# Kernel optimization log

Measured on AMD Instinct MI355X. Metric: run time of the kernel, lower is better.

## Reference

```python
import jax, jax.numpy as jnp
import numpy as np

T, B, U = 256, 4, 64
E_ENC, E_DEC, J, V = 1024, 640, 640, 4096
LN_EPS = 1e-5


def layer_norm(x, gamma, beta):
    mu = jnp.mean(x, axis=-1, keepdims=True)
    var = jnp.mean(jnp.square(x - mu), axis=-1, keepdims=True)
    return (x - mu) * jax.lax.rsqrt(var + LN_EPS) * gamma + beta


def setup_inputs() -> dict:
    key = jax.random.key(0)
    ks = jax.random.split(key, 8)
    inp = {
        "encoder_out": jax.random.normal(ks[0], (T, B, E_ENC), dtype=jnp.float32),
        "decoder_out": jax.random.normal(ks[1], (U, B, E_DEC), dtype=jnp.float32),
        # proj_encoder
        "W_enc": jax.random.normal(ks[2], (J, E_ENC), dtype=jnp.float32) * (E_ENC ** -0.5),
        "b_enc": jnp.zeros((J,), dtype=jnp.float32),
        "g_enc": jnp.ones((J,), dtype=jnp.float32),
        "be_enc": jnp.zeros((J,), dtype=jnp.float32),
        # proj_decoder
        "W_dec": jax.random.normal(ks[3], (J, E_DEC), dtype=jnp.float32) * (E_DEC ** -0.5),
        "b_dec": jnp.zeros((J,), dtype=jnp.float32),
        "g_dec": jnp.ones((J,), dtype=jnp.float32),
        "be_dec": jnp.zeros((J,), dtype=jnp.float32),
        # fc_out (init.normal_ with std = joint_dim**-0.5)
        "W_out": jax.random.normal(ks[4], (V, J), dtype=jnp.float32) * (J ** -0.5),
        "b_out": jnp.zeros((V,), dtype=jnp.float32),
    }
    return inp


def reference(encoder_out, decoder_out, W_enc, b_enc, g_enc, be_enc,
              W_dec, b_dec, g_dec, be_dec, W_out, b_out):
    # encoder_out: [T, B, E_enc] -> project+LN -> transpose -> [B, T, J]
    enc = layer_norm(jnp.einsum('tbe,je->tbj', encoder_out, W_enc) + b_enc,
                     g_enc, be_enc).transpose(1, 0, 2)
    # decoder_out: [U, B, E_dec] -> [B, U, J]
    dec = layer_norm(jnp.einsum('ube,je->ubj', decoder_out, W_dec) + b_dec,
                     g_dec, be_dec).transpose(1, 0, 2)
    # broadcast outer-sum over T x U, then ReLU: [B, T, U, J]
    joint = jax.nn.relu(enc[:, :, None, :] + dec[:, None, :, :])
    # vocab projection: [B, T, U, V]
    return jnp.einsum('btuj,vj->btuv', joint, W_out) + b_out
```

## Files before the change

kernel.cpp:

```cpp
#include <hip/hip_runtime.h>
#include <stdint.h>

#define T_    256
#define B_    4
#define U_    64
#define EENC  1024
#define EDEC  640
#define J_    640
#define V_    4096

typedef unsigned short u16;
typedef unsigned int   u32;
typedef __bf16 bf16x8 __attribute__((ext_vector_type(8)));
typedef short  s16x8  __attribute__((ext_vector_type(8)));
typedef float  f32x4  __attribute__((ext_vector_type(4)));

__device__ __forceinline__ u16 f2bf(float f) {
    u32 u = __builtin_bit_cast(u32, f);
    u = (u + 0x7FFFu + ((u >> 16) & 1u)) >> 16;
    return (u16)u;
}
__device__ __forceinline__ float bf2f(u16 b) {
    return __builtin_bit_cast(float, (u32)b << 16);
}

__global__ __launch_bounds__(256) void cvt_bf16(const float* __restrict__ src,
                                                u16* __restrict__ dst, int n4) {
    int i = blockIdx.x * 256 + threadIdx.x;
    if (i < n4) {
        float4 v = reinterpret_cast<const float4*>(src)[i];
        ushort4 o;
        o.x = f2bf(v.x); o.y = f2bf(v.y); o.z = f2bf(v.z); o.w = f2bf(v.w);
        reinterpret_cast<ushort4*>(dst)[i] = o;
    }
}

__global__ __launch_bounds__(256) void ln_kernel(const float* __restrict__ proj,
                                                 const float* __restrict__ bias,
                                                 const float* __restrict__ gamma,
                                                 const float* __restrict__ beta,
                                                 u16* __restrict__ out,
                                                 int BDIM, int OUTER) {
    int pr = blockIdx.x;
    int b = pr % BDIM, outer = pr / BDIM;
    const float* row = proj + (size_t)pr * J_;
    int tid = threadIdx.x;

    float x0 = row[tid] + bias[tid];
    float x1 = row[tid + 256] + bias[tid + 256];
    float x2 = 0.f;
    bool has3 = (tid < J_ - 512);
    if (has3) x2 = row[tid + 512] + bias[tid + 512];

    float s1 = x0 + x1 + x2;
    float s2 = x0 * x0 + x1 * x1 + x2 * x2;
    for (int off = 32; off; off >>= 1) {
        s1 += __shfl_down(s1, off, 64);
        s2 += __shfl_down(s2, off, 64);
    }
    __shared__ float ws1[4], ws2[4];
    int w = tid >> 6, lane = tid & 63;
    if (lane == 0) { ws1[w] = s1; ws2[w] = s2; }
    __syncthreads();
    float S1 = ws1[0] + ws1[1] + ws1[2] + ws1[3];
    float S2 = ws2[0] + ws2[1] + ws2[2] + ws2[3];
    float mu = S1 * (1.f / J_);
    float var = S2 * (1.f / J_) - mu * mu;
    float inv = 1.0f / sqrtf(var + 1e-5f);

    size_t orow = ((size_t)b * OUTER + outer) * J_;
    out[orow + tid]       = f2bf((x0 - mu) * inv * gamma[tid]       + beta[tid]);
    out[orow + tid + 256] = f2bf((x1 - mu) * inv * gamma[tid + 256] + beta[tid + 256]);
    if (has3)
        out[orow + tid + 512] = f2bf((x2 - mu) * inv * gamma[tid + 512] + beta[tid + 512]);
}

__global__ __launch_bounds__(256) void joint_mat(const u16* __restrict__ encln,
                                                 const u16* __restrict__ decln,
                                                 u16* __restrict__ joint) {
    int g = blockIdx.x * 256 + threadIdx.x;
    int row = g / (J_ / 8);
    int jc = g - row * (J_ / 8);
    int b = row >> 14;
    int t = (row >> 6) & (T_ - 1);
    int u = row & (U_ - 1);
    s16x8 e = *reinterpret_cast<const s16x8*>(encln + ((size_t)(b * T_ + t)) * J_ + jc * 8);
    s16x8 d = *reinterpret_cast<const s16x8*>(decln + ((size_t)(b * U_ + u)) * J_ + jc * 8);
    s16x8 o;
#pragma unroll
    for (int k = 0; k < 8; ++k) {
        float v = bf2f((u16)e[k]) + bf2f((u16)d[k]);
        o[k] = (short)f2bf(fmaxf(v, 0.f));
    }
    *reinterpret_cast<s16x8*>(joint + (size_t)row * J_ + jc * 8) = o;
}

__global__ __launch_bounds__(256) void gemm_bt(const u16* __restrict__ A,
                                               const u16* __restrict__ Bt,
                                               float* __restrict__ C,
                                               const float* __restrict__ bias,
                                               int K, int ldc) {
    __shared__ u16 As[128 * 64];
    __shared__ u16 Bs[128 * 64];
    const int tid = threadIdx.x;
    const int w = tid >> 6, lane = tid & 63;
    const int wr = w >> 1, wc = w & 1;
    const size_t m0 = (size_t)blockIdx.y * 128;
    const size_t n0 = (size_t)blockIdx.x * 128;

    f32x4 acc[4][4] = {};

    const int l3 = lane >> 3;
    const int c8 = (lane & 7) * 8;
    const int nkt = K >> 6;

    for (int kt = 0; kt < nkt; ++kt) {
        if (kt) __syncthreads();
        const int k0 = kt << 6;
#pragma unroll
        for (int i = 0; i < 4; ++i) {
            const int c = w * 4 + i;
            const int r = c * 8 + l3;
            const u16* ga = A  + (m0 + r) * (size_t)K + k0 + c8;
            const u16* gb = Bt + (n0 + r) * (size_t)K + k0 + c8;
            __builtin_amdgcn_global_load_lds(
                (const __attribute__((address_space(1))) void*)ga,
                (__attribute__((address_space(3))) void*)(As + c * 512), 16, 0, 0);
            __builtin_amdgcn_global_load_lds(
                (const __attribute__((address_space(1))) void*)gb,
                (__attribute__((address_space(3))) void*)(Bs + c * 512), 16, 0, 0);
        }
        __syncthreads();

#pragma unroll
        for (int kk = 0; kk < 2; ++kk) {
            bf16x8 af[4], bfr[4];
#pragma unroll
            for (int i = 0; i < 4; ++i) {
                int ra = wr * 64 + i * 16 + (lane & 15);
                af[i] = *reinterpret_cast<const bf16x8*>(As + ra * 64 + kk * 32 + (lane >> 4) * 8);
                int rb = wc * 64 + i * 16 + (lane & 15);
                bfr[i] = *reinterpret_cast<const bf16x8*>(Bs + rb * 64 + kk * 32 + (lane >> 4) * 8);
            }
#pragma unroll
            for (int i = 0; i < 4; ++i)
#pragma unroll
                for (int j = 0; j < 4; ++j)
                    acc[i][j] = __builtin_amdgcn_mfma_f32_16x16x32_bf16(af[i], bfr[j], acc[i][j], 0, 0, 0);
        }
    }

    const int r4 = (lane >> 4) * 4;
    const int cl = lane & 15;
#pragma unroll
    for (int i = 0; i < 4; ++i) {
#pragma unroll
        for (int j = 0; j < 4; ++j) {
            size_t grow = m0 + wr * 64 + i * 16 + r4;
            size_t gcol = n0 + wc * 64 + j * 16 + cl;
            float bv = bias ? bias[gcol] : 0.f;
#pragma unroll
            for (int r = 0; r < 4; ++r)
                C[(grow + r) * (size_t)ldc + gcol] = acc[i][j][r] + bv;
        }
    }
}

#define BKS  32
#define BIGK 640
#define BIGN 4096
#define NTS  (BIGK / BKS)

__global__ __launch_bounds__(512, 4) void gemm_big(const u16* __restrict__ A,
                                                   const u16* __restrict__ Bt,
                                                   float* __restrict__ C,
                                                   const float* __restrict__ bias) {
    __shared__ u16 Abuf[2][128 * BKS];
    __shared__ u16 Bbuf[2][256 * BKS];

    const int tid = threadIdx.x;
    const int w = tid >> 6, lane = tid & 63;
    const int wr = w >> 2, wc = w & 3;
    const int fr = lane & 15, fq = lane >> 4;

    const int lin = blockIdx.x;
    const int xcd = lin & 7;
    const int idx = lin >> 3;
    const size_t m0 = (size_t)(idx >> 1) * 128;
    const size_t n0 = (size_t)(xcd * 2 + (idx & 1)) * 256;

    const int arow = tid >> 2;
    const int aseg = (tid & 3) ^ (arow & 3);
    const u16* aga  = A + (m0 + arow) * (size_t)BIGK + aseg * 8;
    const int bseg = (tid & 3) ^ (arow & 3);
    const u16* bga0 = Bt + (n0 + arow) * (size_t)BIGK + bseg * 8;
    const u16* bga1 = bga0 + (size_t)128 * BIGK;
    const int sdst = w * 512;

    f32x4 acc[4][4] = {};

#define STAGE(buf, k0)                                                             \
    { __builtin_amdgcn_global_load_lds(                                            \
          (const __attribute__((address_space(1))) void*)(aga + (k0)),             \
          (__attribute__((address_space(3))) void*)(&Abuf[buf][sdst]), 16, 0, 0);  \
      __builtin_amdgcn_global_load_lds(                                            \
          (const __attribute__((address_space(1))) void*)(bga0 + (k0)),            \
          (__attribute__((address_space(3))) void*)(&Bbuf[buf][sdst]), 16, 0, 0);  \
      __builtin_amdgcn_global_load_lds(                                            \
          (const __attribute__((address_space(1))) void*)(bga1 + (k0)),            \
          (__attribute__((address_space(3))) void*)(&Bbuf[buf][4096 + sdst]), 16, 0, 0); }

#define RD_A(buf, mi)                                                              \
    (*reinterpret_cast<const bf16x8*>(&Abuf[buf][                                  \
        (wr * 64 + (mi) * 16 + fr) * BKS +                                         \
        (((fq * 16) ^ (((wr * 64 + (mi) * 16 + fr) & 3) << 4)) >> 1)]))
#define RD_B(buf, ni)                                                              \
    (*reinterpret_cast<const bf16x8*>(&Bbuf[buf][                                  \
        (wc * 64 + (ni) * 16 + fr) * BKS +                                         \
        (((fq * 16) ^ (((wc * 64 + (ni) * 16 + fr) & 3) << 4)) >> 1)]))

#define VM0   asm volatile("s_waitcnt vmcnt(0)" ::: "memory")
#define LGKM0 asm volatile("s_waitcnt lgkmcnt(0)" ::: "memory")

    STAGE(0, 0);
    VM0;
    __builtin_amdgcn_s_barrier();

    for (int t = 0; t < NTS; ++t) {
        const int cur = t & 1, nxt = cur ^ 1;
        const bool pf = (t + 1 < NTS);
        bf16x8 af[4], bf[4];

#pragma unroll
        for (int i = 0; i < 4; ++i) af[i] = RD_A(cur, i);
#pragma unroll
        for (int j = 0; j < 4; ++j) bf[j] = RD_B(cur, j);
        if (pf) STAGE(nxt, (t + 1) * BKS);
        LGKM0;
        __builtin_amdgcn_s_setprio(1);
#pragma unroll
        for (int i = 0; i < 4; ++i)
#pragma unroll
            for (int j = 0; j < 4; ++j)
                acc[i][j] = __builtin_amdgcn_mfma_f32_16x16x32_bf16(af[i], bf[j], acc[i][j], 0, 0, 0);
        __builtin_amdgcn_s_setprio(0);
        if (pf) {
            VM0;
            __builtin_amdgcn_s_barrier();
        }
    }

#undef STAGE
#undef RD_A
#undef RD_B
#undef VM0
#undef LGKM0

    const size_t crow0 = m0 + wr * 64 + fq * 4;
    const size_t ccol0 = n0 + wc * 64 + fr;
#pragma unroll
    for (int ni = 0; ni < 4; ++ni) {
        const size_t col = ccol0 + ni * 16;
        const float bv = bias[col];
#pragma unroll
        for (int mi = 0; mi < 4; ++mi) {
            const size_t rbase = crow0 + mi * 16;
#pragma unroll
            for (int r = 0; r < 4; ++r)
                __builtin_nontemporal_store(acc[mi][ni][r] + bv,
                                            &C[(rbase + r) * (size_t)BIGN + col]);
        }
    }
}

static const size_t O_JOINT = 0;
static const size_t O_WOUT  = 83886080;
static const size_t O_ENCLN = 89128960;
static const size_t O_DECLN = 90439680;
static const size_t O_ENCIN = 90767360;
static const size_t O_DECIN = 92864512;
static const size_t O_WENC  = 93192192;
static const size_t O_WDEC  = 94502912;
static const size_t O_EPROJ = 95322112;
static const size_t O_DPROJ = 97943552;
static const size_t WS_NEEDED = 98598912;

extern "C" void kernel_launch(void* const* d_in, const int* in_sizes, int n_in,
                              void* d_out, int out_size, void* d_ws, size_t ws_size,
                              hipStream_t stream) {
    const float* enc   = (const float*)d_in[0];
    const float* dec   = (const float*)d_in[1];
    const float* Wenc  = (const float*)d_in[2];
    const float* benc  = (const float*)d_in[3];
    const float* genc  = (const float*)d_in[4];
    const float* beenc = (const float*)d_in[5];
    const float* Wdec  = (const float*)d_in[6];
    const float* bdec  = (const float*)d_in[7];
    const float* gdec  = (const float*)d_in[8];
    const float* bedec = (const float*)d_in[9];
    const float* Wout  = (const float*)d_in[10];
    const float* bout  = (const float*)d_in[11];
    float* out = (float*)d_out;

    if (ws_size < WS_NEEDED) return;

    char* ws = (char*)d_ws;
    u16* joint  = (u16*)(ws + O_JOINT);
    u16* wout_b = (u16*)(ws + O_WOUT);
    u16* encln  = (u16*)(ws + O_ENCLN);
    u16* decln  = (u16*)(ws + O_DECLN);
    u16* encin  = (u16*)(ws + O_ENCIN);
    u16* decin  = (u16*)(ws + O_DECIN);
    u16* wenc_b = (u16*)(ws + O_WENC);
    u16* wdec_b = (u16*)(ws + O_WDEC);
    float* eproj = (float*)(ws + O_EPROJ);
    float* dproj = (float*)(ws + O_DPROJ);

    cvt_bf16<<<1024, 256, 0, stream>>>(enc,  encin,  (T_ * B_ * EENC) / 4);
    cvt_bf16<<<160,  256, 0, stream>>>(dec,  decin,  (U_ * B_ * EDEC) / 4);
    cvt_bf16<<<640,  256, 0, stream>>>(Wenc, wenc_b, (J_ * EENC) / 4);
    cvt_bf16<<<400,  256, 0, stream>>>(Wdec, wdec_b, (J_ * EDEC) / 4);
    cvt_bf16<<<2560, 256, 0, stream>>>(Wout, wout_b, (V_ * J_) / 4);

    gemm_bt<<<dim3(J_ / 128, (T_ * B_) / 128), 256, 0, stream>>>(encin, wenc_b, eproj, nullptr, EENC, J_);
    gemm_bt<<<dim3(J_ / 128, (U_ * B_) / 128), 256, 0, stream>>>(decin, wdec_b, dproj, nullptr, EDEC, J_);

    ln_kernel<<<T_ * B_, 256, 0, stream>>>(eproj, benc, genc, beenc, encln, B_, T_);
    ln_kernel<<<U_ * B_, 256, 0, stream>>>(dproj, bdec, gdec, bedec, decln, B_, U_);

    joint_mat<<<(B_ * T_ * U_ * (J_ / 8)) / 256, 256, 0, stream>>>(encln, decln, joint);

    gemm_big<<<(B_ * T_ * U_ / 128) * (V_ / 256), 512, 0, stream>>>(joint, wout_b, out, bout);
}
```

Before: 503.4 us.

## Triple-buffer LDS tiles in big GEMM to prefetch two K-steps ahead

After: 502.9 us. Within noise of the previous version (-0.1%).

```diff
diff --git a/kernel.cpp b/kernel.cpp
--- a/kernel.cpp
+++ b/kernel.cpp
@@ -170,13 +170,15 @@
 #define BIGK 640
 #define BIGN 4096
 #define NTS  (BIGK / BKS)
+#define ASZ  (128 * BKS)
+#define BSZ  (256 * BKS)
 
 __global__ __launch_bounds__(512, 4) void gemm_big(const u16* __restrict__ A,
                                                    const u16* __restrict__ Bt,
                                                    float* __restrict__ C,
                                                    const float* __restrict__ bias) {
-    __shared__ u16 Abuf[2][128 * BKS];
-    __shared__ u16 Bbuf[2][256 * BKS];
+    __shared__ u16 Abuf[3 * ASZ];
+    __shared__ u16 Bbuf[3 * BSZ];
 
     const int tid = threadIdx.x;
     const int w = tid >> 6, lane = tid & 63;
@@ -192,50 +194,52 @@
     const int arow = tid >> 2;
     const int aseg = (tid & 3) ^ (arow & 3);
     const u16* aga  = A + (m0 + arow) * (size_t)BIGK + aseg * 8;
-    const int bseg = (tid & 3) ^ (arow & 3);
-    const u16* bga0 = Bt + (n0 + arow) * (size_t)BIGK + bseg * 8;
+    const u16* bga0 = Bt + (n0 + arow) * (size_t)BIGK + aseg * 8;
     const u16* bga1 = bga0 + (size_t)128 * BIGK;
     const int sdst = w * 512;
 
     f32x4 acc[4][4] = {};
 
-#define STAGE(buf, k0)                                                             \
+#define STAGE(bo, k0)                                                              \
     { __builtin_amdgcn_global_load_lds(                                            \
           (const __attribute__((address_space(1))) void*)(aga + (k0)),             \
-          (__attribute__((address_space(3))) void*)(&Abuf[buf][sdst]), 16, 0, 0);  \
+          (__attribute__((address_space(3))) void*)(&Abuf[(bo) * ASZ + sdst]), 16, 0, 0); \
       __builtin_amdgcn_global_load_lds(                                            \
           (const __attribute__((address_space(1))) void*)(bga0 + (k0)),            \
-          (__attribute__((address_space(3))) void*)(&Bbuf[buf][sdst]), 16, 0, 0);  \
+          (__attribute__((address_space(3))) void*)(&Bbuf[(bo) * BSZ + sdst]), 16, 0, 0); \
       __builtin_amdgcn_global_load_lds(                                            \
           (const __attribute__((address_space(1))) void*)(bga1 + (k0)),            \
-          (__attribute__((address_space(3))) void*)(&Bbuf[buf][4096 + sdst]), 16, 0, 0); }
-
-#define RD_A(buf, mi)                                                              \
-    (*reinterpret_cast<const bf16x8*>(&Abuf[buf][                                  \
+          (__attribute__((address_space(3))) void*)(&Bbuf[(bo) * BSZ + 4096 + sdst]), 16, 0, 0); }
+
+#define RD_A(bo, mi)                                                               \
+    (*reinterpret_cast<const bf16x8*>(&Abuf[(bo) * ASZ +                           \
         (wr * 64 + (mi) * 16 + fr) * BKS +                                         \
         (((fq * 16) ^ (((wr * 64 + (mi) * 16 + fr) & 3) << 4)) >> 1)]))
-#define RD_B(buf, ni)                                                              \
-    (*reinterpret_cast<const bf16x8*>(&Bbuf[buf][                                  \
+#define RD_B(bo, ni)                                                               \
+    (*reinterpret_cast<const bf16x8*>(&Bbuf[(bo) * BSZ +                           \
         (wc * 64 + (ni) * 16 + fr) * BKS +                                         \
         (((fq * 16) ^ (((wc * 64 + (ni) * 16 + fr) & 3) << 4)) >> 1)]))
 
+#define VM3   asm volatile("s_waitcnt vmcnt(3)" ::: "memory")
 #define VM0   asm volatile("s_waitcnt vmcnt(0)" ::: "memory")
 #define LGKM0 asm volatile("s_waitcnt lgkmcnt(0)" ::: "memory")
 
     STAGE(0, 0);
-    VM0;
+    STAGE(1, BKS);
+    VM3;
     __builtin_amdgcn_s_barrier();
 
+    int cur = 0;
     for (int t = 0; t < NTS; ++t) {
-        const int cur = t & 1, nxt = cur ^ 1;
-        const bool pf = (t + 1 < NTS);
+        const bool pf2 = (t + 2 < NTS);
+        int nx2 = cur + 2; if (nx2 >= 3) nx2 -= 3;
         bf16x8 af[4], bf[4];
 
 #pragma unroll
         for (int i = 0; i < 4; ++i) af[i] = RD_A(cur, i);
 #pragma unroll
         for (int j = 0; j < 4; ++j) bf[j] = RD_B(cur, j);
-        if (pf) STAGE(nxt, (t + 1) * BKS);
+        if (pf2) STAGE(nx2, (t + 2) * BKS);
         LGKM0;
         __builtin_amdgcn_s_setprio(1);
 #pragma unroll
@@ -244,15 +248,17 @@
             for (int j = 0; j < 4; ++j)
                 acc[i][j] = __builtin_amdgcn_mfma_f32_16x16x32_bf16(af[i], bf[j], acc[i][j], 0, 0, 0);
         __builtin_amdgcn_s_setprio(0);
-        if (pf) {
-            VM0;
+        if (t + 1 < NTS) {
+            if (pf2) VM3; else VM0;
             __builtin_amdgcn_s_barrier();
         }
+        ++cur; if (cur >= 3) cur = 0;
     }
 
 #undef STAGE
 #undef RD_A
 #undef RD_B
+#undef VM3
 #undef VM0
 #undef LGKM0
 
```

## Retile big GEMM to 128x128 blocks with 64-wide K steps and 4 waves

Applied to the files above, without the earlier changes.

Result: no change. 502.8 us (-0.1%).

```diff
diff --git a/kernel.cpp b/kernel.cpp
--- a/kernel.cpp
+++ b/kernel.cpp
@@ -166,58 +166,56 @@
     }
 }
 
-#define BKS  32
+#define BK2  64
 #define BIGK 640
 #define BIGN 4096
-#define NTS  (BIGK / BKS)
-
-__global__ __launch_bounds__(512, 4) void gemm_big(const u16* __restrict__ A,
+#define NT2  (BIGK / BK2)
+#define TSZ  (128 * BK2)
+
+__global__ __launch_bounds__(256, 2) void gemm_big(const u16* __restrict__ A,
                                                    const u16* __restrict__ Bt,
                                                    float* __restrict__ C,
                                                    const float* __restrict__ bias) {
-    __shared__ u16 Abuf[2][128 * BKS];
-    __shared__ u16 Bbuf[2][256 * BKS];
+    __shared__ u16 Ab[2][TSZ];
+    __shared__ u16 Bb[2][TSZ];
 
     const int tid = threadIdx.x;
     const int w = tid >> 6, lane = tid & 63;
-    const int wr = w >> 2, wc = w & 3;
+    const int wr = w >> 1, wc = w & 1;
     const int fr = lane & 15, fq = lane >> 4;
 
     const int lin = blockIdx.x;
     const int xcd = lin & 7;
     const int idx = lin >> 3;
-    const size_t m0 = (size_t)(idx >> 1) * 128;
-    const size_t n0 = (size_t)(xcd * 2 + (idx & 1)) * 256;
-
-    const int arow = tid >> 2;
-    const int aseg = (tid & 3) ^ (arow & 3);
-    const u16* aga  = A + (m0 + arow) * (size_t)BIGK + aseg * 8;
-    const int bseg = (tid & 3) ^ (arow & 3);
-    const u16* bga0 = Bt + (n0 + arow) * (size_t)BIGK + bseg * 8;
-    const u16* bga1 = bga0 + (size_t)128 * BIGK;
-    const int sdst = w * 512;
+    const size_t m0 = (size_t)(idx >> 2) * 128;
+    const size_t n0 = (size_t)(xcd * 4 + (idx & 3)) * 128;
+
+    const int srow = tid >> 3;
+    const int sseg = (tid & 7) ^ (srow & 7);
+    const u16* aga = A  + (m0 + srow) * (size_t)BIGK + sseg * 8;
+    const u16* bga = Bt + (n0 + srow) * (size_t)BIGK + sseg * 8;
 
     f32x4 acc[4][4] = {};
 
 #define STAGE(buf, k0)                                                             \
-    { __builtin_amdgcn_global_load_lds(                                            \
-          (const __attribute__((address_space(1))) void*)(aga + (k0)),             \
-          (__attribute__((address_space(3))) void*)(&Abuf[buf][sdst]), 16, 0, 0);  \
-      __builtin_amdgcn_global_load_lds(                                            \
-          (const __attribute__((address_space(1))) void*)(bga0 + (k0)),            \
-          (__attribute__((address_space(3))) void*)(&Bbuf[buf][sdst]), 16, 0, 0);  \
-      __builtin_amdgcn_global_load_lds(                                            \
-          (const __attribute__((address_space(1))) void*)(bga1 + (k0)),            \
-          (__attribute__((address_space(3))) void*)(&Bbuf[buf][4096 + sdst]), 16, 0, 0); }
-
-#define RD_A(buf, mi)                                                              \
-    (*reinterpret_cast<const bf16x8*>(&Abuf[buf][                                  \
-        (wr * 64 + (mi) * 16 + fr) * BKS +                                         \
-        (((fq * 16) ^ (((wr * 64 + (mi) * 16 + fr) & 3) << 4)) >> 1)]))
-#define RD_B(buf, ni)                                                              \
-    (*reinterpret_cast<const bf16x8*>(&Bbuf[buf][                                  \
-        (wc * 64 + (ni) * 16 + fr) * BKS +                                         \
-        (((fq * 16) ^ (((wc * 64 + (ni) * 16 + fr) & 3) << 4)) >> 1)]))
+    { _Pragma("unroll")                                                            \
+      for (int c = 0; c < 4; ++c) {                                                \
+        __builtin_amdgcn_global_load_lds(                                          \
+            (const __attribute__((address_space(1))) void*)(aga + (size_t)c * 32 * BIGK + (k0)), \
+            (__attribute__((address_space(3))) void*)(&Ab[buf][c * 2048 + tid * 8]), 16, 0, 0);  \
+        __builtin_amdgcn_global_load_lds(                                          \
+            (const __attribute__((address_space(1))) void*)(bga + (size_t)c * 32 * BIGK + (k0)), \
+            (__attribute__((address_space(3))) void*)(&Bb[buf][c * 2048 + tid * 8]), 16, 0, 0);  \
+      } }
+
+#define RD_A(buf, mi, kk)                                                          \
+    (*reinterpret_cast<const bf16x8*>(&Ab[buf][                                    \
+        (wr * 64 + (mi) * 16 + fr) * 64 +                                          \
+        ((((kk) * 4 + fq) ^ ((wr * 64 + (mi) * 16 + fr) & 7)) * 8)]))
+#define RD_B(buf, ni, kk)                                                          \
+    (*reinterpret_cast<const bf16x8*>(&Bb[buf][                                    \
+        (wc * 64 + (ni) * 16 + fr) * 64 +                                          \
+        ((((kk) * 4 + fq) ^ ((wc * 64 + (ni) * 16 + fr) & 7)) * 8)]))
 
 #define VM0   asm volatile("s_waitcnt vmcnt(0)" ::: "memory")
 #define LGKM0 asm volatile("s_waitcnt lgkmcnt(0)" ::: "memory")
@@ -226,23 +224,32 @@
     VM0;
     __builtin_amdgcn_s_barrier();
 
-    for (int t = 0; t < NTS; ++t) {
+    for (int t = 0; t < NT2; ++t) {
         const int cur = t & 1, nxt = cur ^ 1;
-        const bool pf = (t + 1 < NTS);
-        bf16x8 af[4], bf[4];
-
-#pragma unroll
-        for (int i = 0; i < 4; ++i) af[i] = RD_A(cur, i);
-#pragma unroll
-        for (int j = 0; j < 4; ++j) bf[j] = RD_B(cur, j);
-        if (pf) STAGE(nxt, (t + 1) * BKS);
+        const bool pf = (t + 1 < NT2);
+        bf16x8 af0[4], bf0[4], af1[4], bf1[4];
+
+#pragma unroll
+        for (int i = 0; i < 4; ++i) { af0[i] = RD_A(cur, i, 0); }
+#pragma unroll
+        for (int j = 0; j < 4; ++j) { bf0[j] = RD_B(cur, j, 0); }
+#pragma unroll
+        for (int i = 0; i < 4; ++i) { af1[i] = RD_A(cur, i, 1); }
+#pragma unroll
+        for (int j = 0; j < 4; ++j) { bf1[j] = RD_B(cur, j, 1); }
+        if (pf) STAGE(nxt, (t + 1) * BK2);
         LGKM0;
         __builtin_amdgcn_s_setprio(1);
 #pragma unroll
         for (int i = 0; i < 4; ++i)
 #pragma unroll
             for (int j = 0; j < 4; ++j)
-                acc[i][j] = __builtin_amdgcn_mfma_f32_16x16x32_bf16(af[i], bf[j], acc[i][j], 0, 0, 0);
+                acc[i][j] = __builtin_amdgcn_mfma_f32_16x16x32_bf16(af0[i], bf0[j], acc[i][j], 0, 0, 0);
+#pragma unroll
+        for (int i = 0; i < 4; ++i)
+#pragma unroll
+            for (int j = 0; j < 4; ++j)
+                acc[i][j] = __builtin_amdgcn_mfma_f32_16x16x32_bf16(af1[i], bf1[j], acc[i][j], 0, 0, 0);
         __builtin_amdgcn_s_setprio(0);
         if (pf) {
             VM0;
@@ -330,5 +337,5 @@
 
     joint_mat<<<(B_ * T_ * U_ * (J_ / 8)) / 256, 256, 0, stream>>>(encln, decln, joint);
 
-    gemm_big<<<(B_ * T_ * U_ / 128) * (V_ / 256), 512, 0, stream>>>(joint, wout_b, out, bout);
-}
+    gemm_big<<<(B_ * T_ * U_ / 128) * (V_ / 128), 256, 0, stream>>>(joint, wout_b, out, bout);
+}
```
